# Kernel tuning notes

Measured on AMD Instinct MI355X. Metric: run time of the kernel, lower is better.

The kernel has to match this reference:

```python
import jax, jax.numpy as jnp
import numpy as np

N, E = 50000, 400000
FN, FE = 128, 128          # in/out node and edge feature dims
W = 256                     # fnns_width
EPS = 1e-5


def _layer_norm(x, g, b):
    m = x.mean(-1, keepdims=True)
    var = x.var(-1, keepdims=True)
    return (x - m) / jnp.sqrt(var + EPS) * g + b


def _fnn(x, params):
    # FNN applies ReLU after EVERY linear, including the last one.
    for w, b in params:
        x = jax.nn.relu(x @ w + b)
    return x


def setup_inputs() -> dict:
    key = jax.random.key(0)
    ks = jax.random.split(key, 32)
    s = 0.05
    d = {
        'v': jax.random.normal(ks[0], (N, FN), jnp.float32),
        'e': jax.random.normal(ks[1], (E, FE), jnp.float32),
        'edge_index': jax.random.randint(ks[2], (2, E), 0, N, jnp.int32),
        # edge branch: LayerNorm over concat width FE + 2*FN = 384
        'edge_ln_g': jnp.ones((FE + 2 * FN,), jnp.float32),
        'edge_ln_b': jnp.zeros((FE + 2 * FN,), jnp.float32),
        'ew0': jax.random.normal(ks[3], (FE + 2 * FN, W), jnp.float32) * s,
        'eb0': jnp.zeros((W,), jnp.float32),
        'ew1': jax.random.normal(ks[4], (W, W), jnp.float32) * s,
        'eb1': jnp.zeros((W,), jnp.float32),
        'ew2': jax.random.normal(ks[5], (W, FE), jnp.float32) * s,
        'eb2': jnp.zeros((FE,), jnp.float32),
        'edge_linear': jax.random.normal(ks[6], (FE, FE), jnp.float32) * s,
        # node branch: LayerNorm over concat width FE + FN = 256
        'node_ln_g': jnp.ones((FE + FN,), jnp.float32),
        'node_ln_b': jnp.zeros((FE + FN,), jnp.float32),
        'nw0': jax.random.normal(ks[7], (FE + FN, W), jnp.float32) * s,
        'nb0': jnp.zeros((W,), jnp.float32),
        'nw1': jax.random.normal(ks[8], (W, W), jnp.float32) * s,
        'nb1': jnp.zeros((W,), jnp.float32),
        'nw2': jax.random.normal(ks[9], (W, FN), jnp.float32) * s,
        'nb2': jnp.zeros((FN,), jnp.float32),
        'node_linear': jax.random.normal(ks[10], (FN, FN), jnp.float32) * s,
    }
    return d


def reference(v, e, edge_index, edge_ln_g, edge_ln_b, ew0, eb0, ew1, eb1,
              ew2, eb2, edge_linear, node_ln_g, node_ln_b, nw0, nb0, nw1,
              nb1, nw2, nb2, node_linear):
    row, col = edge_index[0], edge_index[1]
    n = v.shape[0]
    # edge update: residual linear + FNN(LayerNorm(concat))
    edge_in = jnp.concatenate([e, v[row], v[col]], axis=-1)  # [E, 384]
    e_new = e @ edge_linear + _fnn(
        _layer_norm(edge_in, edge_ln_g, edge_ln_b),
        [(ew0, eb0), (ew1, eb1), (ew2, eb2)])
    # mean scatter-aggregate over destination nodes (col)
    counts = jax.ops.segment_sum(jnp.ones((e.shape[0],), e.dtype), col,
                                 num_segments=n)
    e_aggr = jax.ops.segment_sum(e_new, col, num_segments=n)
    e_aggr = e_aggr / jnp.clip(counts, 1.0)[:, None]
    # node update
    node_in = jnp.concatenate([e_aggr, v], axis=-1)  # [N, 256]
    v_new = v @ node_linear + _fnn(
        _layer_norm(node_in, node_ln_g, node_ln_b),
        [(nw0, nb0), (nw1, nb1), (nw2, nb2)])
    return (v_new, e_new)
```

## Files before the change

### kernel.cpp

```cpp
#include <hip/hip_runtime.h>

typedef _Float16 f16_t;
typedef f16_t f16x4 __attribute__((ext_vector_type(4)));
typedef f16_t f16x8 __attribute__((ext_vector_type(8)));
typedef float f32x4 __attribute__((ext_vector_type(4)));

#define MFMA16(a, b, c) __builtin_amdgcn_mfma_f32_16x16x32_f16((a), (b), (c), 0, 0, 0)

__device__ __forceinline__ float bfr(float x) { return (float)(__bf16)x; }

__global__ void pack_weights_kernel(
    const float* __restrict__ ew0, const float* __restrict__ ew1,
    const float* __restrict__ ew2, const float* __restrict__ eL,
    const float* __restrict__ nw0, const float* __restrict__ nw1,
    const float* __restrict__ nw2, const float* __restrict__ nL,
    f16_t* __restrict__ dst)
{
    int tid = blockIdx.x * 256 + threadIdx.x;
    int fid = tid >> 6, lane = tid & 63;
    const float* src; int Ncols, foff, doff;
    if (fid < 192)      { src = ew0; Ncols = 256; foff = 0;   doff = 0;      }
    else if (fid < 320) { src = ew1; Ncols = 256; foff = 192; doff = 98304;  }
    else if (fid < 384) { src = ew2; Ncols = 128; foff = 320; doff = 163840; }
    else if (fid < 416) { src = eL;  Ncols = 128; foff = 384; doff = 196608; }
    else if (fid < 544) { src = nw0; Ncols = 256; foff = 416; doff = 212992; }
    else if (fid < 672) { src = nw1; Ncols = 256; foff = 544; doff = 278528; }
    else if (fid < 736) { src = nw2; Ncols = 128; foff = 672; doff = 344064; }
    else                { src = nL;  Ncols = 128; foff = 736; doff = 376832; }
    int f = fid - foff;
    int NT = Ncols >> 4;
    int kstep = f / NT, ntile = f - kstep * NT;
    int col = ntile * 16 + (lane & 15);
    int kbase = kstep * 32 + ((lane >> 4) << 3);
    f16x8 out;
    #pragma unroll
    for (int j = 0; j < 8; ++j)
        out[j] = (f16_t)bfr(src[(size_t)(kbase + j) * Ncols + col]);
    *reinterpret_cast<f16x8*>(dst + (size_t)doff + ((size_t)f * 64 + lane) * 8) = out;
}

__launch_bounds__(512, 6)
__global__ void edge_kernel(
    const float* __restrict__ vfeat, const float* __restrict__ efeat,
    const int* __restrict__ eidx,
    const float* __restrict__ lng, const float* __restrict__ lnb,
    const f16_t* __restrict__ pw,
    const float* __restrict__ b0, const float* __restrict__ b1,
    const float* __restrict__ b2,
    float* __restrict__ out_e, float* __restrict__ aggr, float* __restrict__ cnts,
    int Ee)
{
    __shared__ f16_t X[32 * 392];
    __shared__ f16_t H1[32 * 264];
    __shared__ f16_t ER[32 * 136];
    __shared__ int cidx[32];

    const int t    = threadIdx.x;
    const int lane = t & 63;
    const int wv   = t >> 6;
    const size_t ebase = (size_t)blockIdx.x * 32;

    const int el = t >> 4;
    const int pp = t & 15;
    const size_t eg = ebase + el;
    const int r0 = eidx[eg];
    const int c0 = eidx[(size_t)Ee + eg];

    float4 d[6];
    float s = 0.f, sq = 0.f;
    {
        const float4* e4 = (const float4*)efeat;
        const float4* v4 = (const float4*)vfeat;
        #pragma unroll
        for (int i = 0; i < 6; ++i) {
            int q = i * 16 + pp;
            float4 r;
            if (q < 32)      r = e4[eg * 32 + q];
            else if (q < 64) r = v4[(size_t)r0 * 32 + (q - 32)];
            else             r = v4[(size_t)c0 * 32 + (q - 64)];
            d[i].x = bfr(r.x); d[i].y = bfr(r.y); d[i].z = bfr(r.z); d[i].w = bfr(r.w);
            if (q < 32) {
                f16x4 ev;
                ev[0] = (f16_t)d[i].x; ev[1] = (f16_t)d[i].y;
                ev[2] = (f16_t)d[i].z; ev[3] = (f16_t)d[i].w;
                *reinterpret_cast<f16x4*>(&ER[el * 136 + q * 4]) = ev;
            }
            s  += d[i].x + d[i].y + d[i].z + d[i].w;
            sq += d[i].x*d[i].x + d[i].y*d[i].y + d[i].z*d[i].z + d[i].w*d[i].w;
        }
        if (pp == 0) {
            cidx[el] = c0;
            unsafeAtomicAdd(&cnts[c0], 1.0f);
        }
    }
    #pragma unroll
    for (int off = 1; off < 16; off <<= 1) {
        s  += __shfl_xor(s, off);
        sq += __shfl_xor(sq, off);
    }
    const float mean = s * (1.f / 384.f);
    const float rstd = 1.f / sqrtf(sq * (1.f / 384.f) - mean * mean + 1e-5f);

    {
        const float4* g4p = (const float4*)lng;
        const float4* bpp = (const float4*)lnb;
        #pragma unroll
        for (int i = 0; i < 6; ++i) {
            int q = i * 16 + pp;
            float4 g = g4p[q]; float4 bb = bpp[q];
            f16x4 y;
            y[0] = (f16_t)((d[i].x - mean) * rstd * bfr(g.x) + bfr(bb.x));
            y[1] = (f16_t)((d[i].y - mean) * rstd * bfr(g.y) + bfr(bb.y));
            y[2] = (f16_t)((d[i].z - mean) * rstd * bfr(g.z) + bfr(bb.z));
            y[3] = (f16_t)((d[i].w - mean) * rstd * bfr(g.w) + bfr(bb.w));
            *reinterpret_cast<f16x4*>(&X[el * 392 + q * 4]) = y;
        }
    }
    __syncthreads();

    const int r16 = lane & 15;
    const int g4i = lane >> 4;

    {
        f32x4 acc[2][2] = {};
        const f16_t* bw = pw;
        #pragma unroll
        for (int ks = 0; ks < 12; ++ks) {
            f16x8 a0 = *reinterpret_cast<const f16x8*>(&X[r16 * 392 + ks * 32 + g4i * 8]);
            f16x8 a1 = *reinterpret_cast<const f16x8*>(&X[(16 + r16) * 392 + ks * 32 + g4i * 8]);
            #pragma unroll
            for (int n = 0; n < 2; ++n) {
                f16x8 b = *reinterpret_cast<const f16x8*>(
                    &bw[((size_t)(ks * 16 + wv * 2 + n) * 64 + lane) * 8]);
                acc[0][n] = MFMA16(a0, b, acc[0][n]);
                acc[1][n] = MFMA16(a1, b, acc[1][n]);
            }
        }
        #pragma unroll
        for (int n = 0; n < 2; ++n) {
            int c = wv * 32 + n * 16 + r16;
            float bias = bfr(b0[c]);
            #pragma unroll
            for (int m = 0; m < 2; ++m)
                #pragma unroll
                for (int qi = 0; qi < 4; ++qi) {
                    int rr = m * 16 + g4i * 4 + qi;
                    H1[rr * 264 + c] = (f16_t)fmaxf(acc[m][n][qi] + bias, 0.f);
                }
        }
    }
    __syncthreads();

    f16_t* h2 = X;
    {
        f32x4 acc[2][2] = {};
        const f16_t* bw = pw + 98304;
        #pragma unroll
        for (int ks = 0; ks < 8; ++ks) {
            f16x8 a0 = *reinterpret_cast<const f16x8*>(&H1[r16 * 264 + ks * 32 + g4i * 8]);
            f16x8 a1 = *reinterpret_cast<const f16x8*>(&H1[(16 + r16) * 264 + ks * 32 + g4i * 8]);
            #pragma unroll
            for (int n = 0; n < 2; ++n) {
                f16x8 b = *reinterpret_cast<const f16x8*>(
                    &bw[((size_t)(ks * 16 + wv * 2 + n) * 64 + lane) * 8]);
                acc[0][n] = MFMA16(a0, b, acc[0][n]);
                acc[1][n] = MFMA16(a1, b, acc[1][n]);
            }
        }
        #pragma unroll
        for (int n = 0; n < 2; ++n) {
            int c = wv * 32 + n * 16 + r16;
            float bias = bfr(b1[c]);
            #pragma unroll
            for (int m = 0; m < 2; ++m)
                #pragma unroll
                for (int qi = 0; qi < 4; ++qi) {
                    int rr = m * 16 + g4i * 4 + qi;
                    h2[rr * 264 + c] = (f16_t)fmaxf(acc[m][n][qi] + bias, 0.f);
                }
        }
    }
    __syncthreads();

    {
        f32x4 accF[2] = {}, accR[2] = {};
        const f16_t* bw = pw + 163840;
        #pragma unroll
        for (int ks = 0; ks < 8; ++ks) {
            f16x8 a0 = *reinterpret_cast<const f16x8*>(&h2[r16 * 264 + ks * 32 + g4i * 8]);
            f16x8 a1 = *reinterpret_cast<const f16x8*>(&h2[(16 + r16) * 264 + ks * 32 + g4i * 8]);
            f16x8 b = *reinterpret_cast<const f16x8*>(
                &bw[((size_t)(ks * 8 + wv) * 64 + lane) * 8]);
            accF[0] = MFMA16(a0, b, accF[0]);
            accF[1] = MFMA16(a1, b, accF[1]);
        }
        const f16_t* bwL = pw + 196608;
        #pragma unroll
        for (int ks = 0; ks < 4; ++ks) {
            f16x8 a0 = *reinterpret_cast<const f16x8*>(&ER[r16 * 136 + ks * 32 + g4i * 8]);
            f16x8 a1 = *reinterpret_cast<const f16x8*>(&ER[(16 + r16) * 136 + ks * 32 + g4i * 8]);
            f16x8 b = *reinterpret_cast<const f16x8*>(
                &bwL[((size_t)(ks * 8 + wv) * 64 + lane) * 8]);
            accR[0] = MFMA16(a0, b, accR[0]);
            accR[1] = MFMA16(a1, b, accR[1]);
        }
        int c = wv * 16 + r16;
        float bias = bfr(b2[c]);
        #pragma unroll
        for (int m = 0; m < 2; ++m)
            #pragma unroll
            for (int qi = 0; qi < 4; ++qi) {
                int rr = m * 16 + g4i * 4 + qi;
                float val = accR[m][qi] + fmaxf(accF[m][qi] + bias, 0.f);
                size_t eg2 = ebase + rr;
                out_e[eg2 * 128 + c] = val;
                unsafeAtomicAdd(&aggr[(size_t)cidx[rr] * 128 + c], val);
            }
    }
}

__launch_bounds__(512, 6)
__global__ void node_kernel(
    const float* __restrict__ vfeat, const float* __restrict__ aggr,
    const float* __restrict__ cnts,
    const float* __restrict__ lng, const float* __restrict__ lnb,
    const f16_t* __restrict__ pw,
    const float* __restrict__ b0, const float* __restrict__ b1,
    const float* __restrict__ b2,
    float* __restrict__ out_v, int Nn)
{
    __shared__ f16_t X[32 * 264];
    __shared__ f16_t H1[32 * 264];

    const int t    = threadIdx.x;
    const int lane = t & 63;
    const int wv   = t >> 6;
    const size_t nbase = (size_t)blockIdx.x * 32;

    const int nl = t >> 4;
    const int pp = t & 15;
    const size_t ng = nbase + nl;
    const bool valid = ng < (size_t)Nn;

    float4 d[4];
    float s = 0.f, sq = 0.f;
    {
        float cmax = 1.f;
        if (valid) cmax = fmaxf(cnts[ng], 1.f);
        const float4* a4 = (const float4*)aggr;
        const float4* v4 = (const float4*)vfeat;
        #pragma unroll
        for (int i = 0; i < 4; ++i) {
            int q = i * 16 + pp;
            float4 r = make_float4(0.f, 0.f, 0.f, 0.f);
            if (valid) {
                if (q < 32) {
                    r = a4[ng * 32 + q];
                    r.x = r.x / cmax; r.y = r.y / cmax;
                    r.z = r.z / cmax; r.w = r.w / cmax;
                } else {
                    float4 rv = v4[ng * 32 + (q - 32)];
                    r.x = bfr(rv.x); r.y = bfr(rv.y); r.z = bfr(rv.z); r.w = bfr(rv.w);
                }
            }
            d[i] = r;
            s  += r.x + r.y + r.z + r.w;
            sq += r.x*r.x + r.y*r.y + r.z*r.z + r.w*r.w;
        }
    }
    #pragma unroll
    for (int off = 1; off < 16; off <<= 1) {
        s  += __shfl_xor(s, off);
        sq += __shfl_xor(sq, off);
    }
    const float mean = s * (1.f / 256.f);
    const float rstd = 1.f / sqrtf(sq * (1.f / 256.f) - mean * mean + 1e-5f);
    {
        const float4* g4p = (const float4*)lng;
        const float4* bpp = (const float4*)lnb;
        #pragma unroll
        for (int i = 0; i < 4; ++i) {
            int q = i * 16 + pp;
            float4 g = g4p[q]; float4 bb = bpp[q];
            f16x4 y;
            y[0] = (f16_t)((d[i].x - mean) * rstd * bfr(g.x) + bfr(bb.x));
            y[1] = (f16_t)((d[i].y - mean) * rstd * bfr(g.y) + bfr(bb.y));
            y[2] = (f16_t)((d[i].z - mean) * rstd * bfr(g.z) + bfr(bb.z));
            y[3] = (f16_t)((d[i].w - mean) * rstd * bfr(g.w) + bfr(bb.w));
            *reinterpret_cast<f16x4*>(&X[nl * 264 + q * 4]) = y;
        }
    }
    __syncthreads();

    const int r16 = lane & 15;
    const int g4i = lane >> 4;

    {
        f32x4 acc[2][2] = {};
        const f16_t* bw = pw;
        #pragma unroll
        for (int ks = 0; ks < 8; ++ks) {
            f16x8 a0 = *reinterpret_cast<const f16x8*>(&X[r16 * 264 + ks * 32 + g4i * 8]);
            f16x8 a1 = *reinterpret_cast<const f16x8*>(&X[(16 + r16) * 264 + ks * 32 + g4i * 8]);
            #pragma unroll
            for (int n = 0; n < 2; ++n) {
                f16x8 b = *reinterpret_cast<const f16x8*>(
                    &bw[((size_t)(ks * 16 + wv * 2 + n) * 64 + lane) * 8]);
                acc[0][n] = MFMA16(a0, b, acc[0][n]);
                acc[1][n] = MFMA16(a1, b, acc[1][n]);
            }
        }
        #pragma unroll
        for (int n = 0; n < 2; ++n) {
            int c = wv * 32 + n * 16 + r16;
            float bias = bfr(b0[c]);
            #pragma unroll
            for (int m = 0; m < 2; ++m)
                #pragma unroll
                for (int qi = 0; qi < 4; ++qi) {
                    int rr = m * 16 + g4i * 4 + qi;
                    H1[rr * 264 + c] = (f16_t)fmaxf(acc[m][n][qi] + bias, 0.f);
                }
        }
    }
    __syncthreads();

    f16_t* h2 = X;
    {
        f32x4 acc[2][2] = {};
        const f16_t* bw = pw + 65536;
        #pragma unroll
        for (int ks = 0; ks < 8; ++ks) {
            f16x8 a0 = *reinterpret_cast<const f16x8*>(&H1[r16 * 264 + ks * 32 + g4i * 8]);
            f16x8 a1 = *reinterpret_cast<const f16x8*>(&H1[(16 + r16) * 264 + ks * 32 + g4i * 8]);
            #pragma unroll
            for (int n = 0; n < 2; ++n) {
                f16x8 b = *reinterpret_cast<const f16x8*>(
                    &bw[((size_t)(ks * 16 + wv * 2 + n) * 64 + lane) * 8]);
                acc[0][n] = MFMA16(a0, b, acc[0][n]);
                acc[1][n] = MFMA16(a1, b, acc[1][n]);
            }
        }
        #pragma unroll
        for (int n = 0; n < 2; ++n) {
            int c = wv * 32 + n * 16 + r16;
            float bias = bfr(b1[c]);
            #pragma unroll
            for (int m = 0; m < 2; ++m)
                #pragma unroll
                for (int qi = 0; qi < 4; ++qi) {
                    int rr = m * 16 + g4i * 4 + qi;
                    h2[rr * 264 + c] = (f16_t)fmaxf(acc[m][n][qi] + bias, 0.f);
                }
        }
    }
    __syncthreads();

    {
        f32x4 accF[2] = {}, accR[2] = {};
        const f16_t* bw = pw + 131072;
        #pragma unroll
        for (int ks = 0; ks < 8; ++ks) {
            f16x8 a0 = *reinterpret_cast<const f16x8*>(&h2[r16 * 264 + ks * 32 + g4i * 8]);
            f16x8 a1 = *reinterpret_cast<const f16x8*>(&h2[(16 + r16) * 264 + ks * 32 + g4i * 8]);
            f16x8 b = *reinterpret_cast<const f16x8*>(
                &bw[((size_t)(ks * 8 + wv) * 64 + lane) * 8]);
            accF[0] = MFMA16(a0, b, accF[0]);
            accF[1] = MFMA16(a1, b, accF[1]);
        }
        const f16_t* bwL = pw + 163840;
        #pragma unroll
        for (int ks = 0; ks < 4; ++ks) {
            f16x8 a[2];
            #pragma unroll
            for (int m = 0; m < 2; ++m) {
                size_t rv = nbase + (size_t)(m * 16 + r16);
                if (rv >= (size_t)Nn) rv = (size_t)Nn - 1;
                const float* src = &vfeat[rv * 128 + ks * 32 + g4i * 8];
                float4 f0 = *(const float4*)src;
                float4 f1 = *(const float4*)(src + 4);
                f16x8 av;
                av[0] = (f16_t)bfr(f0.x); av[1] = (f16_t)bfr(f0.y);
                av[2] = (f16_t)bfr(f0.z); av[3] = (f16_t)bfr(f0.w);
                av[4] = (f16_t)bfr(f1.x); av[5] = (f16_t)bfr(f1.y);
                av[6] = (f16_t)bfr(f1.z); av[7] = (f16_t)bfr(f1.w);
                a[m] = av;
            }
            f16x8 b = *reinterpret_cast<const f16x8*>(
                &bwL[((size_t)(ks * 8 + wv) * 64 + lane) * 8]);
            accR[0] = MFMA16(a[0], b, accR[0]);
            accR[1] = MFMA16(a[1], b, accR[1]);
        }
        int c = wv * 16 + r16;
        float bias = bfr(b2[c]);
        #pragma unroll
        for (int m = 0; m < 2; ++m)
            #pragma unroll
            for (int qi = 0; qi < 4; ++qi) {
                int rr = m * 16 + g4i * 4 + qi;
                size_t ng2 = nbase + rr;
                if (ng2 < (size_t)Nn) {
                    float val = accR[m][qi] + fmaxf(accF[m][qi] + bias, 0.f);
                    out_v[ng2 * 128 + c] = val;
                }
            }
    }
}

extern "C" void kernel_launch(void* const* d_in, const int* in_sizes, int n_in,
                              void* d_out, int out_size, void* d_ws, size_t ws_size,
                              hipStream_t stream)
{
    const float* v    = (const float*)d_in[0];
    const float* e    = (const float*)d_in[1];
    const int*   eidx = (const int*)d_in[2];
    const float* elng = (const float*)d_in[3];
    const float* elnb = (const float*)d_in[4];
    const float* ew0  = (const float*)d_in[5];
    const float* eb0  = (const float*)d_in[6];
    const float* ew1  = (const float*)d_in[7];
    const float* eb1  = (const float*)d_in[8];
    const float* ew2  = (const float*)d_in[9];
    const float* eb2  = (const float*)d_in[10];
    const float* eLin = (const float*)d_in[11];
    const float* nlng = (const float*)d_in[12];
    const float* nlnb = (const float*)d_in[13];
    const float* nw0  = (const float*)d_in[14];
    const float* nb0  = (const float*)d_in[15];
    const float* nw1  = (const float*)d_in[16];
    const float* nb1  = (const float*)d_in[17];
    const float* nw2  = (const float*)d_in[18];
    const float* nb2  = (const float*)d_in[19];
    const float* nLin = (const float*)d_in[20];

    const int Nn = in_sizes[0] / 128;
    const int Ee = in_sizes[1] / 128;

    float* out_v = (float*)d_out;
    float* out_e = out_v + (size_t)Nn * 128;

    float* aggr = (float*)d_ws;
    float* cnts = aggr + (size_t)Nn * 128;
    f16_t* packw = (f16_t*)((char*)d_ws + (size_t)Nn * 129 * 4);

    hipMemsetAsync(d_ws, 0, (size_t)Nn * 129 * 4, stream);

    pack_weights_kernel<<<192, 256, 0, stream>>>(ew0, ew1, ew2, eLin,
                                                 nw0, nw1, nw2, nLin, packw);

    edge_kernel<<<Ee / 32, 512, 0, stream>>>(v, e, eidx, elng, elnb, packw,
                                             eb0, eb1, eb2, out_e, aggr, cnts, Ee);

    node_kernel<<<(Nn + 31) / 32, 512, 0, stream>>>(v, aggr, cnts, nlng, nlnb,
                                                    packw + 212992, nb0, nb1, nb2,
                                                    out_v, Nn);
}
```

Baseline: 453.5 us.

## Use 64-edge tiles with 1024 threads and in-place LDS reuse in edge kernel

Result: faster. 436.0 us (-3.9%).

```diff
diff --git a/kernel.cpp b/kernel.cpp
--- a/kernel.cpp
+++ b/kernel.cpp
@@ -39,7 +39,7 @@
     *reinterpret_cast<f16x8*>(dst + (size_t)doff + ((size_t)f * 64 + lane) * 8) = out;
 }
 
-__launch_bounds__(512, 6)
+__launch_bounds__(1024, 8)
 __global__ void edge_kernel(
     const float* __restrict__ vfeat, const float* __restrict__ efeat,
     const int* __restrict__ eidx,
@@ -50,15 +50,14 @@
     float* __restrict__ out_e, float* __restrict__ aggr, float* __restrict__ cnts,
     int Ee)
 {
-    __shared__ f16_t X[32 * 392];
-    __shared__ f16_t H1[32 * 264];
-    __shared__ f16_t ER[32 * 136];
-    __shared__ int cidx[32];
+    __shared__ f16_t X[64 * 392];
+    __shared__ f16_t ER[64 * 136];
+    __shared__ int cidx[64];
 
     const int t    = threadIdx.x;
     const int lane = t & 63;
     const int wv   = t >> 6;
-    const size_t ebase = (size_t)blockIdx.x * 32;
+    const size_t ebase = (size_t)blockIdx.x * 64;
 
     const int el = t >> 4;
     const int pp = t & 15;
@@ -66,7 +65,6 @@
     const int r0 = eidx[eg];
     const int c0 = eidx[(size_t)Ee + eg];
 
-    float4 d[6];
     float s = 0.f, sq = 0.f;
     {
         const float4* e4 = (const float4*)efeat;
@@ -78,15 +76,14 @@
             if (q < 32)      r = e4[eg * 32 + q];
             else if (q < 64) r = v4[(size_t)r0 * 32 + (q - 32)];
             else             r = v4[(size_t)c0 * 32 + (q - 64)];
-            d[i].x = bfr(r.x); d[i].y = bfr(r.y); d[i].z = bfr(r.z); d[i].w = bfr(r.w);
-            if (q < 32) {
-                f16x4 ev;
-                ev[0] = (f16_t)d[i].x; ev[1] = (f16_t)d[i].y;
-                ev[2] = (f16_t)d[i].z; ev[3] = (f16_t)d[i].w;
-                *reinterpret_cast<f16x4*>(&ER[el * 136 + q * 4]) = ev;
-            }
-            s  += d[i].x + d[i].y + d[i].z + d[i].w;
-            sq += d[i].x*d[i].x + d[i].y*d[i].y + d[i].z*d[i].z + d[i].w*d[i].w;
+            r.x = bfr(r.x); r.y = bfr(r.y); r.z = bfr(r.z); r.w = bfr(r.w);
+            f16x4 h;
+            h[0] = (f16_t)r.x; h[1] = (f16_t)r.y; h[2] = (f16_t)r.z; h[3] = (f16_t)r.w;
+            *reinterpret_cast<f16x4*>(&X[el * 392 + q * 4]) = h;
+            if (q < 32)
+                *reinterpret_cast<f16x4*>(&ER[el * 136 + q * 4]) = h;
+            s  += r.x + r.y + r.z + r.w;
+            sq += r.x*r.x + r.y*r.y + r.z*r.z + r.w*r.w;
         }
         if (pp == 0) {
             cidx[el] = c0;
@@ -107,13 +104,13 @@
         #pragma unroll
         for (int i = 0; i < 6; ++i) {
             int q = i * 16 + pp;
+            f16x4 h = *reinterpret_cast<f16x4*>(&X[el * 392 + q * 4]);
             float4 g = g4p[q]; float4 bb = bpp[q];
-            f16x4 y;
-            y[0] = (f16_t)((d[i].x - mean) * rstd * bfr(g.x) + bfr(bb.x));
-            y[1] = (f16_t)((d[i].y - mean) * rstd * bfr(g.y) + bfr(bb.y));
-            y[2] = (f16_t)((d[i].z - mean) * rstd * bfr(g.z) + bfr(bb.z));
-            y[3] = (f16_t)((d[i].w - mean) * rstd * bfr(g.w) + bfr(bb.w));
-            *reinterpret_cast<f16x4*>(&X[el * 392 + q * 4]) = y;
+            h[0] = (f16_t)(((float)h[0] - mean) * rstd * bfr(g.x) + bfr(bb.x));
+            h[1] = (f16_t)(((float)h[1] - mean) * rstd * bfr(g.y) + bfr(bb.y));
+            h[2] = (f16_t)(((float)h[2] - mean) * rstd * bfr(g.z) + bfr(bb.z));
+            h[3] = (f16_t)(((float)h[3] - mean) * rstd * bfr(g.w) + bfr(bb.w));
+            *reinterpret_cast<f16x4*>(&X[el * 392 + q * 4]) = h;
         }
     }
     __syncthreads();
@@ -122,95 +119,94 @@
     const int g4i = lane >> 4;
 
     {
-        f32x4 acc[2][2] = {};
+        f32x4 acc[4] = {};
         const f16_t* bw = pw;
         #pragma unroll
         for (int ks = 0; ks < 12; ++ks) {
-            f16x8 a0 = *reinterpret_cast<const f16x8*>(&X[r16 * 392 + ks * 32 + g4i * 8]);
-            f16x8 a1 = *reinterpret_cast<const f16x8*>(&X[(16 + r16) * 392 + ks * 32 + g4i * 8]);
-            #pragma unroll
-            for (int n = 0; n < 2; ++n) {
-                f16x8 b = *reinterpret_cast<const f16x8*>(
-                    &bw[((size_t)(ks * 16 + wv * 2 + n) * 64 + lane) * 8]);
-                acc[0][n] = MFMA16(a0, b, acc[0][n]);
-                acc[1][n] = MFMA16(a1, b, acc[1][n]);
-            }
-        }
-        #pragma unroll
-        for (int n = 0; n < 2; ++n) {
-            int c = wv * 32 + n * 16 + r16;
-            float bias = bfr(b0[c]);
-            #pragma unroll
-            for (int m = 0; m < 2; ++m)
-                #pragma unroll
-                for (int qi = 0; qi < 4; ++qi) {
-                    int rr = m * 16 + g4i * 4 + qi;
-                    H1[rr * 264 + c] = (f16_t)fmaxf(acc[m][n][qi] + bias, 0.f);
-                }
-        }
-    }
-    __syncthreads();
-
-    f16_t* h2 = X;
-    {
-        f32x4 acc[2][2] = {};
+            f16x8 b = *reinterpret_cast<const f16x8*>(
+                &bw[((size_t)(ks * 16 + wv) * 64 + lane) * 8]);
+            #pragma unroll
+            for (int m = 0; m < 4; ++m) {
+                f16x8 a = *reinterpret_cast<const f16x8*>(
+                    &X[(m * 16 + r16) * 392 + ks * 32 + g4i * 8]);
+                acc[m] = MFMA16(a, b, acc[m]);
+            }
+        }
+        __syncthreads();
+        int c = wv * 16 + r16;
+        float bias = bfr(b0[c]);
+        #pragma unroll
+        for (int m = 0; m < 4; ++m)
+            #pragma unroll
+            for (int qi = 0; qi < 4; ++qi) {
+                int rr = m * 16 + g4i * 4 + qi;
+                X[rr * 264 + c] = (f16_t)fmaxf(acc[m][qi] + bias, 0.f);
+            }
+    }
+    __syncthreads();
+
+    {
+        f32x4 acc[4] = {};
         const f16_t* bw = pw + 98304;
         #pragma unroll
         for (int ks = 0; ks < 8; ++ks) {
-            f16x8 a0 = *reinterpret_cast<const f16x8*>(&H1[r16 * 264 + ks * 32 + g4i * 8]);
-            f16x8 a1 = *reinterpret_cast<const f16x8*>(&H1[(16 + r16) * 264 + ks * 32 + g4i * 8]);
-            #pragma unroll
-            for (int n = 0; n < 2; ++n) {
-                f16x8 b = *reinterpret_cast<const f16x8*>(
-                    &bw[((size_t)(ks * 16 + wv * 2 + n) * 64 + lane) * 8]);
-                acc[0][n] = MFMA16(a0, b, acc[0][n]);
-                acc[1][n] = MFMA16(a1, b, acc[1][n]);
-            }
-        }
-        #pragma unroll
-        for (int n = 0; n < 2; ++n) {
-            int c = wv * 32 + n * 16 + r16;
-            float bias = bfr(b1[c]);
-            #pragma unroll
-            for (int m = 0; m < 2; ++m)
-                #pragma unroll
-                for (int qi = 0; qi < 4; ++qi) {
-                    int rr = m * 16 + g4i * 4 + qi;
-                    h2[rr * 264 + c] = (f16_t)fmaxf(acc[m][n][qi] + bias, 0.f);
-                }
-        }
-    }
-    __syncthreads();
-
-    {
+            f16x8 b = *reinterpret_cast<const f16x8*>(
+                &bw[((size_t)(ks * 16 + wv) * 64 + lane) * 8]);
+            #pragma unroll
+            for (int m = 0; m < 4; ++m) {
+                f16x8 a = *reinterpret_cast<const f16x8*>(
+                    &X[(m * 16 + r16) * 264 + ks * 32 + g4i * 8]);
+                acc[m] = MFMA16(a, b, acc[m]);
+            }
+        }
+        __syncthreads();
+        int c = wv * 16 + r16;
+        float bias = bfr(b1[c]);
+        #pragma unroll
+        for (int m = 0; m < 4; ++m)
+            #pragma unroll
+            for (int qi = 0; qi < 4; ++qi) {
+                int rr = m * 16 + g4i * 4 + qi;
+                X[rr * 264 + c] = (f16_t)fmaxf(acc[m][qi] + bias, 0.f);
+            }
+    }
+    __syncthreads();
+
+    {
+        const int nh = wv & 7;
+        const int mh = wv >> 3;
         f32x4 accF[2] = {}, accR[2] = {};
         const f16_t* bw = pw + 163840;
         #pragma unroll
         for (int ks = 0; ks < 8; ++ks) {
-            f16x8 a0 = *reinterpret_cast<const f16x8*>(&h2[r16 * 264 + ks * 32 + g4i * 8]);
-            f16x8 a1 = *reinterpret_cast<const f16x8*>(&h2[(16 + r16) * 264 + ks * 32 + g4i * 8]);
-            f16x8 b = *reinterpret_cast<const f16x8*>(
-                &bw[((size_t)(ks * 8 + wv) * 64 + lane) * 8]);
-            accF[0] = MFMA16(a0, b, accF[0]);
-            accF[1] = MFMA16(a1, b, accF[1]);
+            f16x8 b = *reinterpret_cast<const f16x8*>(
+                &bw[((size_t)(ks * 8 + nh) * 64 + lane) * 8]);
+            #pragma unroll
+            for (int m = 0; m < 2; ++m) {
+                f16x8 a = *reinterpret_cast<const f16x8*>(
+                    &X[(mh * 32 + m * 16 + r16) * 264 + ks * 32 + g4i * 8]);
+                accF[m] = MFMA16(a, b, accF[m]);
+            }
         }
         const f16_t* bwL = pw + 196608;
         #pragma unroll
         for (int ks = 0; ks < 4; ++ks) {
-            f16x8 a0 = *reinterpret_cast<const f16x8*>(&ER[r16 * 136 + ks * 32 + g4i * 8]);
-            f16x8 a1 = *reinterpret_cast<const f16x8*>(&ER[(16 + r16) * 136 + ks * 32 + g4i * 8]);
-            f16x8 b = *reinterpret_cast<const f16x8*>(
-                &bwL[((size_t)(ks * 8 + wv) * 64 + lane) * 8]);
-            accR[0] = MFMA16(a0, b, accR[0]);
-            accR[1] = MFMA16(a1, b, accR[1]);
-        }
-        int c = wv * 16 + r16;
+            f16x8 b = *reinterpret_cast<const f16x8*>(
+                &bwL[((size_t)(ks * 8 + nh) * 64 + lane) * 8]);
+            #pragma unroll
+            for (int m = 0; m < 2; ++m) {
+                f16x8 a = *reinterpret_cast<const f16x8*>(
+                    &ER[(mh * 32 + m * 16 + r16) * 136 + ks * 32 + g4i * 8]);
+                accR[m] = MFMA16(a, b, accR[m]);
+            }
+        }
+        int c = nh * 16 + r16;
         float bias = bfr(b2[c]);
         #pragma unroll
         for (int m = 0; m < 2; ++m)
             #pragma unroll
             for (int qi = 0; qi < 4; ++qi) {
-                int rr = m * 16 + g4i * 4 + qi;
+                int rr = mh * 32 + m * 16 + g4i * 4 + qi;
                 float val = accR[m][qi] + fmaxf(accF[m][qi] + bias, 0.f);
                 size_t eg2 = ebase + rr;
                 out_e[eg2 * 128 + c] = val;
@@ -341,6 +337,7 @@
                 acc[1][n] = MFMA16(a1, b, acc[1][n]);
             }
         }
+        __syncthreads();
         #pragma unroll
         for (int n = 0; n < 2; ++n) {
             int c = wv * 32 + n * 16 + r16;
@@ -448,8 +445,8 @@
     pack_weights_kernel<<<192, 256, 0, stream>>>(ew0, ew1, ew2, eLin,
                                                  nw0, nw1, nw2, nLin, packw);
 
-    edge_kernel<<<Ee / 32, 512, 0, stream>>>(v, e, eidx, elng, elnb, packw,
-                                             eb0, eb1, eb2, out_e, aggr, cnts, Ee);
+    edge_kernel<<<(Ee + 63) / 64, 1024, 0, stream>>>(v, e, eidx, elng, elnb, packw,
+                                                     eb0, eb1, eb2, out_e, aggr, cnts, Ee);
 
     node_kernel<<<(Nn + 31) / 32, 512, 0, stream>>>(v, aggr, cnts, nlng, nlnb,
                                                     packw + 212992, nb0, nb1, nb2,
```
